# Performance work log

Hardware: AMD Instinct MI355X
Metric: run time of the kernel (lower is better)

Reference implementation:

```python
import jax, jax.numpy as jnp
import numpy as np

N = 100_000   # total nodes in batched graph
E = 800_000   # total edges
D = 64        # in_dim
H = 64        # hidden_dim
C = 10        # out_dim (num classes)
L = 3         # num_layers
G = 500       # graphs in batch
EPS = 1e-5    # BatchNorm eps


def setup_inputs() -> dict:
    key = jax.random.key(0)
    ks = jax.random.split(key, 12)
    feat = jax.random.normal(ks[0], (N, D), dtype=jnp.float32)
    src = jax.random.randint(ks[1], (E,), 0, N, dtype=jnp.int32)
    dst = jax.random.randint(ks[2], (E,), 0, N, dtype=jnp.int32)
    node2graph = jnp.sort(jax.random.randint(ks[3], (N,), 0, G, dtype=jnp.int32))
    # stacked GCN layer params (in_dim == hidden_dim so all layers share shape)
    Ws = jax.random.normal(ks[4], (L, H, H), dtype=jnp.float32) * 0.1
    bs = jax.random.normal(ks[5], (L, H), dtype=jnp.float32) * 0.01
    gammas = 1.0 + 0.1 * jax.random.normal(ks[6], (L, H), dtype=jnp.float32)
    betas = 0.1 * jax.random.normal(ks[7], (L, H), dtype=jnp.float32)
    means = 0.1 * jax.random.normal(ks[8], (L, H), dtype=jnp.float32)
    vars_ = jax.random.uniform(ks[9], (L, H), dtype=jnp.float32) + 0.5
    Wc = jax.random.normal(ks[10], (H, C), dtype=jnp.float32) * 0.1
    bc = jax.random.normal(ks[11], (C,), dtype=jnp.float32) * 0.01
    return {"feat": feat, "src": src, "dst": dst, "node2graph": node2graph,
            "Ws": Ws, "bs": bs, "gammas": gammas, "betas": betas,
            "means": means, "vars_": vars_, "Wc": Wc, "bc": bc}


def reference(feat, src, dst, node2graph, Ws, bs, gammas, betas, means, vars_, Wc, bc):
    h = feat
    for l in range(L):
        # dgl copy_src + sum: aggregate source features at destination nodes
        m = jax.ops.segment_sum(h[src], dst, num_segments=N)  # [N, H]
        h = m @ Ws[l] + bs[l]                                  # Linear
        # BatchNorm1d (eval mode, running stats)
        h = (h - means[l]) * (gammas[l] / jnp.sqrt(vars_[l] + EPS)) + betas[l]
        h = jax.nn.elu(h)
    logits = h @ Wc + bc                    # classify(h)
    logp = jax.nn.log_softmax(logits, axis=1)
    Hent = -jnp.sum(jnp.exp(logp) * logp, axis=1)   # entropy per node
    lam = 1.0 - Hent / jnp.max(Hent)                # lambda_list
    # ragged per-graph weighted sum pooling
    pooled = jax.ops.segment_sum(lam[:, None] * h, node2graph, num_segments=G)  # [G, H]
    return pooled @ Wc + bc                 # final classify (dropout eval = id)
```

## Files before the change

kernel.cpp:

```cpp
#include <hip/hip_runtime.h>
#include <hip/hip_bf16.h>
#include <math.h>

#define NNODES 100000
#define NEDGES 800000
#define HDIM 64
#define CDIM 10
#define NGRAPH 500
#define CAP 24
#define OVFCAP 16384
#define BN_EPS 1e-5f
#define TN 64

typedef __attribute__((ext_vector_type(8))) short short8;
typedef __attribute__((ext_vector_type(4))) float f32x4;

__device__ __forceinline__ float bflo(unsigned u){ return __uint_as_float(u << 16); }
__device__ __forceinline__ float bfhi(unsigned u){ return __uint_as_float(u & 0xFFFF0000u); }
__device__ __forceinline__ unsigned f2bf(float f){
    unsigned u = __float_as_uint(f);
    u += 0x7FFFu + ((u >> 16) & 1u);
    return u >> 16;
}

__global__ void prep_fill(const float4* __restrict__ F, uint4* __restrict__ B,
                          const int* __restrict__ src, const int* __restrict__ dst,
                          unsigned* __restrict__ cnt, int* __restrict__ csr,
                          unsigned* __restrict__ ovfcnt, int* __restrict__ ovf) {
    int i = blockIdx.x * 256 + threadIdx.x;
    float4 a = F[2*i], b = F[2*i+1];
    uint4 o;
    o.x = f2bf(a.x) | (f2bf(a.y) << 16);
    o.y = f2bf(a.z) | (f2bf(a.w) << 16);
    o.z = f2bf(b.x) | (f2bf(b.y) << 16);
    o.w = f2bf(b.z) | (f2bf(b.w) << 16);
    B[i] = o;
    int d = dst[i], s = src[i];
    unsigned slot = atomicAdd(&cnt[d], 1u);
    if (slot < CAP) {
        csr[(size_t)d * CAP + slot] = s;
    } else {
        unsigned oo = atomicAdd(ovfcnt, 1u);
        if (oo < OVFCAP) { ovf[2*oo] = s; ovf[2*oo+1] = d; }
    }
}

template<int LAYER>
__global__ __launch_bounds__(512, 4) void layer_fused(
        const unsigned* __restrict__ hb, const unsigned* __restrict__ cnt,
        const int* __restrict__ csr, const unsigned* __restrict__ ovfcnt,
        const int* __restrict__ ovf,
        const float* __restrict__ Ws, const float* __restrict__ bs,
        const float* __restrict__ gammas, const float* __restrict__ betas,
        const float* __restrict__ means, const float* __restrict__ vars_,
        unsigned short* __restrict__ out16) {
    __shared__ unsigned short Mb[TN][72];
    __shared__ unsigned short Wt[HDIM][72];
    __shared__ float Scl[HDIM], Shl[HDIM];
    int tid = threadIdx.x;
    int base = blockIdx.x * TN;

    const float* Wg = Ws + (size_t)LAYER*HDIM*HDIM;
    #pragma unroll
    for (int r = 0; r < 8; ++r) {
        int f = tid + 512*r;
        int k = f >> 6, c = f & 63;
        Wt[c][k] = (unsigned short)f2bf(Wg[f]);
    }
    if (tid < HDIM) {
        int c = tid;
        float b  = bs[LAYER*HDIM + c];
        float gm = gammas[LAYER*HDIM + c];
        float be = betas[LAYER*HDIM + c];
        float mu = means[LAYER*HDIM + c];
        float vv = vars_[LAYER*HDIM + c];
        float s  = gm * rsqrtf(vv + BN_EPS);
        Scl[c] = s;
        Shl[c] = (b - mu) * s + be;
    }

    int row = tid >> 3;
    int sub = tid & 7;
    int node = base + row;
    const uint4* h4 = (const uint4*)hb;
    unsigned novf = *ovfcnt; if (novf > OVFCAP) novf = OVFCAP;
    {
        float a0=0,a1=0,a2=0,a3=0,a4=0,a5=0,a6=0,a7=0;
        if (node < NNODES) {
            unsigned deg = cnt[node]; if (deg > CAP) deg = CAP;
            const int* ed = csr + (size_t)node * CAP;
            unsigned e = 0;
            for (; e + 4 <= deg; e += 4) {
                int4 iv = *(const int4*)(ed + e);
                uint4 v0 = h4[(size_t)iv.x*8 + sub];
                uint4 v1 = h4[(size_t)iv.y*8 + sub];
                uint4 v2 = h4[(size_t)iv.z*8 + sub];
                uint4 v3 = h4[(size_t)iv.w*8 + sub];
                a0 += bflo(v0.x)+bflo(v1.x)+bflo(v2.x)+bflo(v3.x);
                a1 += bfhi(v0.x)+bfhi(v1.x)+bfhi(v2.x)+bfhi(v3.x);
                a2 += bflo(v0.y)+bflo(v1.y)+bflo(v2.y)+bflo(v3.y);
                a3 += bfhi(v0.y)+bfhi(v1.y)+bfhi(v2.y)+bfhi(v3.y);
                a4 += bflo(v0.z)+bflo(v1.z)+bflo(v2.z)+bflo(v3.z);
                a5 += bfhi(v0.z)+bfhi(v1.z)+bfhi(v2.z)+bfhi(v3.z);
                a6 += bflo(v0.w)+bflo(v1.w)+bflo(v2.w)+bflo(v3.w);
                a7 += bfhi(v0.w)+bfhi(v1.w)+bfhi(v2.w)+bfhi(v3.w);
            }
            for (; e < deg; ++e) {
                uint4 v = h4[(size_t)ed[e]*8 + sub];
                a0 += bflo(v.x); a1 += bfhi(v.x);
                a2 += bflo(v.y); a3 += bfhi(v.y);
                a4 += bflo(v.z); a5 += bfhi(v.z);
                a6 += bflo(v.w); a7 += bfhi(v.w);
            }
            if (novf) {
                for (unsigned o = 0; o < novf; ++o) {
                    if (ovf[2*o+1] == node) {
                        uint4 v = h4[(size_t)ovf[2*o]*8 + sub];
                        a0 += bflo(v.x); a1 += bfhi(v.x);
                        a2 += bflo(v.y); a3 += bfhi(v.y);
                        a4 += bflo(v.z); a5 += bfhi(v.z);
                        a6 += bflo(v.w); a7 += bfhi(v.w);
                    }
                }
            }
        }
        uint4 pk;
        pk.x = f2bf(a0) | (f2bf(a1) << 16);
        pk.y = f2bf(a2) | (f2bf(a3) << 16);
        pk.z = f2bf(a4) | (f2bf(a5) << 16);
        pk.w = f2bf(a6) | (f2bf(a7) << 16);
        *(uint4*)&Mb[row][sub*8] = pk;
    }
    __syncthreads();

    int w  = tid >> 6;
    if (w < 4) {
        int l  = tid & 63;
        int lr = l & 15;
        int lq = l >> 4;
        short8 a0 = *(const short8*)&Mb[w*16 + lr][lq*8];
        short8 a1 = *(const short8*)&Mb[w*16 + lr][32 + lq*8];
        f32x4 acc0 = {0.f,0.f,0.f,0.f}, acc1 = acc0, acc2 = acc0, acc3 = acc0;
        {
            short8 b0 = *(const short8*)&Wt[ 0 + lr][lq*8];
            short8 b1 = *(const short8*)&Wt[ 0 + lr][32 + lq*8];
            acc0 = __builtin_amdgcn_mfma_f32_16x16x32_bf16(a0, b0, acc0, 0, 0, 0);
            acc0 = __builtin_amdgcn_mfma_f32_16x16x32_bf16(a1, b1, acc0, 0, 0, 0);
        }
        {
            short8 b0 = *(const short8*)&Wt[16 + lr][lq*8];
            short8 b1 = *(const short8*)&Wt[16 + lr][32 + lq*8];
            acc1 = __builtin_amdgcn_mfma_f32_16x16x32_bf16(a0, b0, acc1, 0, 0, 0);
            acc1 = __builtin_amdgcn_mfma_f32_16x16x32_bf16(a1, b1, acc1, 0, 0, 0);
        }
        {
            short8 b0 = *(const short8*)&Wt[32 + lr][lq*8];
            short8 b1 = *(const short8*)&Wt[32 + lr][32 + lq*8];
            acc2 = __builtin_amdgcn_mfma_f32_16x16x32_bf16(a0, b0, acc2, 0, 0, 0);
            acc2 = __builtin_amdgcn_mfma_f32_16x16x32_bf16(a1, b1, acc2, 0, 0, 0);
        }
        {
            short8 b0 = *(const short8*)&Wt[48 + lr][lq*8];
            short8 b1 = *(const short8*)&Wt[48 + lr][32 + lq*8];
            acc3 = __builtin_amdgcn_mfma_f32_16x16x32_bf16(a0, b0, acc3, 0, 0, 0);
            acc3 = __builtin_amdgcn_mfma_f32_16x16x32_bf16(a1, b1, acc3, 0, 0, 0);
        }

        #pragma unroll
        for (int t = 0; t < 4; ++t) {
            f32x4 a = (t==0)?acc0:(t==1)?acc1:(t==2)?acc2:acc3;
            int col = t*16 + lr;
            float s = Scl[col], sh = Shl[col];
            #pragma unroll
            for (int r = 0; r < 4; ++r) {
                int n2 = base + w*16 + lq*4 + r;
                if (n2 < NNODES) {
                    float y = a[r]*s + sh;
                    y = (y > 0.f) ? y : expm1f(y);
                    out16[(size_t)n2*HDIM + col] = (unsigned short)f2bf(y);
                }
            }
        }
    }
}

__global__ __launch_bounds__(256) void classify_bf16(
        const uint4* __restrict__ h4, const float* __restrict__ Wc,
        const float* __restrict__ bc, float* __restrict__ Hent,
        unsigned* __restrict__ maxH) {
    __shared__ float Wl[HDIM*11];
    __shared__ float bl[CDIM];
    __shared__ float wmax[4];
    int tid = threadIdx.x;
    for (int idx = tid; idx < HDIM*CDIM; idx += 256)
        Wl[(idx/CDIM)*11 + (idx%CDIM)] = Wc[idx];
    if (tid < CDIM) bl[tid] = bc[tid];
    __syncthreads();

    int node = blockIdx.x * 32 + (tid >> 3);
    int sub  = tid & 7;
    uint4 v = h4[(size_t)node*8 + sub];
    float h[8];
    h[0]=bflo(v.x); h[1]=bfhi(v.x); h[2]=bflo(v.y); h[3]=bfhi(v.y);
    h[4]=bflo(v.z); h[5]=bfhi(v.z); h[6]=bflo(v.w); h[7]=bfhi(v.w);

    float lg[CDIM];
    #pragma unroll
    for (int c = 0; c < CDIM; ++c) lg[c] = 0.f;
    #pragma unroll
    for (int k = 0; k < 8; ++k) {
        const float* wr = &Wl[(sub*8 + k)*11];
        float x = h[k];
        #pragma unroll
        for (int c = 0; c < CDIM; ++c) lg[c] += x * wr[c];
    }
    #pragma unroll
    for (int m = 1; m < 8; m <<= 1)
        #pragma unroll
        for (int c = 0; c < CDIM; ++c) lg[c] += __shfl_xor(lg[c], m, 64);
    #pragma unroll
    for (int c = 0; c < CDIM; ++c) lg[c] += bl[c];

    float mx = lg[0];
    #pragma unroll
    for (int c = 1; c < CDIM; ++c) mx = fmaxf(mx, lg[c]);
    float se = 0.f, dot = 0.f;
    #pragma unroll
    for (int c = 0; c < CDIM; ++c) { float e = expf(lg[c]-mx); se += e; dot += e*lg[c]; }
    float Hv = (mx + logf(se)) - dot/se;
    Hv = fmaxf(Hv, 0.f);
    if (sub == 0) Hent[node] = Hv;

    float m8 = Hv;
    #pragma unroll
    for (int m = 8; m < 64; m <<= 1) m8 = fmaxf(m8, __shfl_xor(m8, m, 64));
    if ((tid & 63) == 0) wmax[tid >> 6] = m8;
    __syncthreads();
    if (tid == 0) {
        float mm = fmaxf(fmaxf(wmax[0], wmax[1]), fmaxf(wmax[2], wmax[3]));
        atomicMax(maxH, __float_as_uint(mm));
    }
}

__global__ void pool_final_bf16(const unsigned* __restrict__ H2, const float* __restrict__ Hent,
                                const unsigned* __restrict__ maxH, const int* __restrict__ n2g,
                                const float* __restrict__ Wc, const float* __restrict__ bc,
                                float* __restrict__ out) {
    __shared__ float partial[8][HDIM];
    __shared__ float pooled[HDIM];
    int g = blockIdx.x;
    int tid = threadIdx.x;

    int lo = 0, hi = NNODES;
    while (lo < hi) { int mid = (lo+hi) >> 1; if (n2g[mid] < g) lo = mid+1; else hi = mid; }
    int start = lo;
    hi = NNODES;
    while (lo < hi) { int mid = (lo+hi) >> 1; if (n2g[mid] < g+1) lo = mid+1; else hi = mid; }
    int end = lo;

    float invMax = 1.0f / __uint_as_float(*maxH);
    int half = tid >> 5, l = tid & 31;
    float ax = 0.f, ay = 0.f;
    for (int i = start + half; i < end; i += 8) {
        float lam = 1.0f - Hent[i] * invMax;
        unsigned u = H2[(size_t)i*32 + l];
        ax += lam * bflo(u);
        ay += lam * bfhi(u);
    }
    partial[half][2*l]   = ax;
    partial[half][2*l+1] = ay;
    __syncthreads();
    if (tid < HDIM) {
        float s = 0.f;
        #pragma unroll
        for (int hh = 0; hh < 8; ++hh) s += partial[hh][tid];
        pooled[tid] = s;
    }
    __syncthreads();
    if (tid < CDIM) {
        float s = bc[tid];
        for (int k = 0; k < HDIM; ++k) s += pooled[k] * Wc[k*CDIM + tid];
        out[g*CDIM + tid] = s;
    }
}

extern "C" void kernel_launch(void* const* d_in, const int* in_sizes, int n_in,
                              void* d_out, int out_size, void* d_ws, size_t ws_size,
                              hipStream_t stream) {
    const float* feat  = (const float*)d_in[0];
    const int*   src   = (const int*)d_in[1];
    const int*   dst   = (const int*)d_in[2];
    const int*   n2g   = (const int*)d_in[3];
    const float* Ws    = (const float*)d_in[4];
    const float* bs    = (const float*)d_in[5];
    const float* gam   = (const float*)d_in[6];
    const float* bet   = (const float*)d_in[7];
    const float* mea   = (const float*)d_in[8];
    const float* var_  = (const float*)d_in[9];
    const float* Wc    = (const float*)d_in[10];
    const float* bc    = (const float*)d_in[11];
    float* out = (float*)d_out;

    char* ws = (char*)d_ws;
    size_t off = 0;
    auto take = [&](size_t bytes) {
        char* p = ws + off;
        off += (bytes + 255) & ~(size_t)255;
        return p;
    };

    unsigned* cnt    = (unsigned*)take((size_t)NNODES*4);
    unsigned* ovfcnt = (unsigned*)take(4);
    unsigned* maxH   = (unsigned*)take(4);
    int*      ovf    = (int*)take((size_t)OVFCAP*2*4);
    float*    Hent   = (float*)take((size_t)NNODES*4);
    unsigned* featb  = (unsigned*)take((size_t)NNODES*HDIM*2);
    unsigned* HA     = (unsigned*)take((size_t)NNODES*HDIM*2);
    unsigned* HB     = (unsigned*)take((size_t)NNODES*HDIM*2);
    int*      csr    = (int*)take((size_t)NNODES*CAP*4);

    hipMemsetAsync(cnt, 0, (size_t)NNODES*4, stream);
    hipMemsetAsync(ovfcnt, 0, 4, stream);
    hipMemsetAsync(maxH, 0, 4, stream);

    prep_fill<<<NEDGES/256, 256, 0, stream>>>((const float4*)feat, (uint4*)featb,
                                              src, dst, cnt, csr, ovfcnt, ovf);

    int grid = (NNODES + TN - 1) / TN;
    layer_fused<0><<<grid, 512, 0, stream>>>(featb, cnt, csr, ovfcnt, ovf,
                                             Ws, bs, gam, bet, mea, var_, (unsigned short*)HA);
    layer_fused<1><<<grid, 512, 0, stream>>>((const unsigned*)HA, cnt, csr, ovfcnt, ovf,
                                             Ws, bs, gam, bet, mea, var_, (unsigned short*)HB);
    layer_fused<2><<<grid, 512, 0, stream>>>((const unsigned*)HB, cnt, csr, ovfcnt, ovf,
                                             Ws, bs, gam, bet, mea, var_, (unsigned short*)HA);

    classify_bf16<<<(NNODES+31)/32, 256, 0, stream>>>((const uint4*)HA, Wc, bc, Hent, maxH);
    pool_final_bf16<<<NGRAPH, 256, 0, stream>>>(HA, Hent, maxH, n2g, Wc, bc, out);
}
```

Baseline: 191.8 us.

## Build CSR via two-pass binned partition instead of global atomics

Replaces the single-pass edge scatter, which used one global atomic per edge on per-node counters, with a two-stage build. Edges are first binned by destination range using shared-memory histograms and one global atomic per bin per block. A second kernel then builds per-node slot lists in LDS and writes them out coalesced. This aims to remove contended scattered global atomics and uncoalesced CSR writes, at the cost of an extra kernel launch and an intermediate bin buffer. Each bin block is read four times by the second pass.

```diff
diff --git a/kernel.cpp b/kernel.cpp
--- a/kernel.cpp
+++ b/kernel.cpp
@@ -11,6 +11,11 @@
 #define OVFCAP 16384
 #define BN_EPS 1e-5f
 #define TN 64
+#define EBLK 2048
+#define NBIN2 49
+#define BINCAP2 20480
+#define SUBN 512
+#define NBLKB 196
 
 typedef __attribute__((ext_vector_type(8))) short short8;
 typedef __attribute__((ext_vector_type(4))) float f32x4;
@@ -23,26 +28,91 @@
     return u >> 16;
 }
 
-__global__ void prep_fill(const float4* __restrict__ F, uint4* __restrict__ B,
-                          const int* __restrict__ src, const int* __restrict__ dst,
-                          unsigned* __restrict__ cnt, int* __restrict__ csr,
-                          unsigned* __restrict__ ovfcnt, int* __restrict__ ovf) {
-    int i = blockIdx.x * 256 + threadIdx.x;
-    float4 a = F[2*i], b = F[2*i+1];
-    uint4 o;
-    o.x = f2bf(a.x) | (f2bf(a.y) << 16);
-    o.y = f2bf(a.z) | (f2bf(a.w) << 16);
-    o.z = f2bf(b.x) | (f2bf(b.y) << 16);
-    o.w = f2bf(b.z) | (f2bf(b.w) << 16);
-    B[i] = o;
-    int d = dst[i], s = src[i];
-    unsigned slot = atomicAdd(&cnt[d], 1u);
-    if (slot < CAP) {
-        csr[(size_t)d * CAP + slot] = s;
-    } else {
-        unsigned oo = atomicAdd(ovfcnt, 1u);
-        if (oo < OVFCAP) { ovf[2*oo] = s; ovf[2*oo+1] = d; }
-    }
+__global__ __launch_bounds__(256) void prep_part(
+        const float4* __restrict__ F, uint4* __restrict__ B,
+        const int* __restrict__ src, const int* __restrict__ dst,
+        unsigned* __restrict__ gcur, unsigned* __restrict__ bin_edges,
+        unsigned* __restrict__ ovfcnt, int* __restrict__ ovf) {
+    __shared__ unsigned hist[64], basev[64], loc[64];
+    int t = threadIdx.x, blk = blockIdx.x;
+    if (t < 64) { hist[t] = 0; loc[t] = 0; }
+    __syncthreads();
+
+    unsigned pk[8]; int bn[8];
+    #pragma unroll
+    for (int i = 0; i < 8; ++i) {
+        int e = blk*EBLK + i*256 + t;
+        if (e < NEDGES) {
+            int d = dst[e], s = src[e];
+            bn[i] = d >> 11;
+            pk[i] = ((unsigned)(d & 2047) << 17) | (unsigned)s;
+            atomicAdd(&hist[bn[i]], 1u);
+        } else bn[i] = -1;
+        if (e < NEDGES) {
+            float4 a = F[2*(size_t)e], b = F[2*(size_t)e+1];
+            uint4 o;
+            o.x = f2bf(a.x) | (f2bf(a.y) << 16);
+            o.y = f2bf(a.z) | (f2bf(a.w) << 16);
+            o.z = f2bf(b.x) | (f2bf(b.y) << 16);
+            o.w = f2bf(b.z) | (f2bf(b.w) << 16);
+            B[e] = o;
+        }
+    }
+    __syncthreads();
+    if (t < 64 && hist[t]) basev[t] = atomicAdd(&gcur[t], hist[t]);
+    __syncthreads();
+    #pragma unroll
+    for (int i = 0; i < 8; ++i) {
+        if (bn[i] >= 0) {
+            unsigned p = basev[bn[i]] + atomicAdd(&loc[bn[i]], 1u);
+            if (p < BINCAP2) bin_edges[(size_t)bn[i]*BINCAP2 + p] = pk[i];
+            else {
+                unsigned oo = atomicAdd(ovfcnt, 1u);
+                if (oo < OVFCAP) {
+                    ovf[2*oo]   = (int)(pk[i] & 0x1FFFFu);
+                    ovf[2*oo+1] = (bn[i] << 11) | (int)(pk[i] >> 17);
+                }
+            }
+        }
+    }
+}
+
+__global__ __launch_bounds__(256) void build_csr2(
+        const unsigned* __restrict__ gcur, const unsigned* __restrict__ bin_edges,
+        unsigned* __restrict__ cnt, int* __restrict__ csr,
+        unsigned* __restrict__ ovfcnt, int* __restrict__ ovf) {
+    __shared__ unsigned lcnt[SUBN];
+    __shared__ __align__(16) int lcsr[SUBN][CAP];
+    int b = blockIdx.x, t = threadIdx.x;
+    int node0 = b * SUBN;
+    int bin = node0 >> 11;
+    unsigned q = (unsigned)(node0 >> 9) & 3u;
+    for (int i = t; i < SUBN; i += 256) lcnt[i] = 0;
+    __syncthreads();
+    unsigned ec = gcur[bin]; if (ec > BINCAP2) ec = BINCAP2;
+    const unsigned* be = bin_edges + (size_t)bin*BINCAP2;
+    for (unsigned i = t; i < ec; i += 256) {
+        unsigned u = be[i];
+        unsigned dl = u >> 17;
+        if ((dl >> 9) == q) {
+            unsigned ln = dl & 511u;
+            int s = (int)(u & 0x1FFFFu);
+            unsigned slot = atomicAdd(&lcnt[ln], 1u);
+            if (slot < CAP) lcsr[ln][slot] = s;
+            else {
+                unsigned oo = atomicAdd(ovfcnt, 1u);
+                if (oo < OVFCAP) { ovf[2*oo] = s; ovf[2*oo+1] = node0 + (int)ln; }
+            }
+        }
+    }
+    __syncthreads();
+    for (int i = t; i < SUBN; i += 256) {
+        int node = node0 + i;
+        if (node < NNODES) cnt[node] = lcnt[i];
+    }
+    const uint4* ls = (const uint4*)&lcsr[0][0];
+    uint4* gs = (uint4*)(csr + (size_t)node0 * CAP);
+    for (int i = t; i < SUBN*CAP/4; i += 256) gs[i] = ls[i];
 }
 
 template<int LAYER>
@@ -133,7 +203,7 @@
     }
     __syncthreads();
 
-    int w  = tid >> 6;
+    int w = tid >> 6;
     if (w < 4) {
         int l  = tid & 63;
         int lr = l & 15;
@@ -167,9 +237,9 @@
         }
 
         #pragma unroll
-        for (int t = 0; t < 4; ++t) {
-            f32x4 a = (t==0)?acc0:(t==1)?acc1:(t==2)?acc2:acc3;
-            int col = t*16 + lr;
+        for (int tt = 0; tt < 4; ++tt) {
+            f32x4 a = (tt==0)?acc0:(tt==1)?acc1:(tt==2)?acc2:acc3;
+            int col = tt*16 + lr;
             float s = Scl[col], sh = Shl[col];
             #pragma unroll
             for (int r = 0; r < 4; ++r) {
@@ -309,22 +379,25 @@
         return p;
     };
 
-    unsigned* cnt    = (unsigned*)take((size_t)NNODES*4);
-    unsigned* ovfcnt = (unsigned*)take(4);
-    unsigned* maxH   = (unsigned*)take(4);
-    int*      ovf    = (int*)take((size_t)OVFCAP*2*4);
-    float*    Hent   = (float*)take((size_t)NNODES*4);
-    unsigned* featb  = (unsigned*)take((size_t)NNODES*HDIM*2);
-    unsigned* HA     = (unsigned*)take((size_t)NNODES*HDIM*2);
-    unsigned* HB     = (unsigned*)take((size_t)NNODES*HDIM*2);
-    int*      csr    = (int*)take((size_t)NNODES*CAP*4);
-
-    hipMemsetAsync(cnt, 0, (size_t)NNODES*4, stream);
+    unsigned* gcur     = (unsigned*)take((size_t)64*4);
+    unsigned* ovfcnt   = (unsigned*)take(4);
+    unsigned* maxH     = (unsigned*)take(4);
+    int*      ovf      = (int*)take((size_t)OVFCAP*2*4);
+    unsigned* cnt      = (unsigned*)take((size_t)NNODES*4);
+    float*    Hent     = (float*)take((size_t)NNODES*4);
+    unsigned* featb    = (unsigned*)take((size_t)NNODES*HDIM*2);
+    unsigned* HA       = (unsigned*)take((size_t)NNODES*HDIM*2);
+    unsigned* HB       = (unsigned*)take((size_t)NNODES*HDIM*2);
+    unsigned* bin_edges= (unsigned*)take((size_t)NBIN2*BINCAP2*4);
+    int*      csr      = (int*)take((size_t)NBLKB*SUBN*CAP*4);
+
+    hipMemsetAsync(gcur, 0, 64*4, stream);
     hipMemsetAsync(ovfcnt, 0, 4, stream);
     hipMemsetAsync(maxH, 0, 4, stream);
 
-    prep_fill<<<NEDGES/256, 256, 0, stream>>>((const float4*)feat, (uint4*)featb,
-                                              src, dst, cnt, csr, ovfcnt, ovf);
+    prep_part<<<(NEDGES + EBLK - 1)/EBLK, 256, 0, stream>>>(
+        (const float4*)feat, (uint4*)featb, src, dst, gcur, bin_edges, ovfcnt, ovf);
+    build_csr2<<<NBLKB, 256, 0, stream>>>(gcur, bin_edges, cnt, csr, ovfcnt, ovf);
 
     int grid = (NNODES + TN - 1) / TN;
     layer_fused<0><<<grid, 512, 0, stream>>>(featb, cnt, csr, ovfcnt, ovf,
```

New measurement: 189.4 us. No clear change (-1.2%).
